# Kernel tuning notes

Measured on AMD Instinct MI355X. Metric: run time of the kernel, lower is better.

The kernel has to match this reference:

```python
import jax, jax.numpy as jnp
import numpy as np

B, D, N, S = 1024, 512, 500000, 32768


def setup_inputs() -> dict:
    key = jax.random.key(0)
    k1, k2, k3 = jax.random.split(key, 3)
    inputs = jax.random.normal(k1, (B, D), dtype=jnp.float32)
    # Linear(D, N) init: uniform(-0.05, 0.05) weight, zero bias
    weight = jax.random.uniform(k2, (N, D), dtype=jnp.float32, minval=-0.05, maxval=0.05)
    bias = jnp.zeros((N,), dtype=jnp.float32)
    sample_ids = jax.random.randint(k3, (S,), 0, N, dtype=jnp.int64)
    return {"inputs": inputs, "weight": weight, "bias": bias, "sample_ids": sample_ids}


def reference(inputs, weight, bias, sample_ids):
    # Gather retrieved class embeddings: [S, D] and their biases [S]
    sample_weights = weight[sample_ids]
    sample_bias = bias[sample_ids]
    # Sampled logits: inputs @ sample_weights.T + bias  -> [B, S]
    # (matches sample_weights.matmul(inputs.t()).t() + sample_bias in torch)
    logits = jnp.einsum("bd,sd->bs", inputs, sample_weights) + sample_bias
    return logits
```

## Files before the change

kernel.cpp:

```cpp
#include <hip/hip_runtime.h>
#include <stdint.h>

#define B_DIM 1024
#define D_DIM 512
#define S_DIM 32768

typedef __attribute__((ext_vector_type(8))) short bf16x8;
typedef __attribute__((ext_vector_type(4))) float f32x4;
typedef __attribute__((ext_vector_type(8))) unsigned short u16x8;

#define AS1 __attribute__((address_space(1)))
#define AS3 __attribute__((address_space(3)))

__device__ __forceinline__ unsigned short f2bf(float f) {
  union { float f; uint32_t u; } x; x.f = f;
  uint32_t r = x.u + 0x7fffu + ((x.u >> 16) & 1u);
  return (unsigned short)(r >> 16);
}

__global__ __launch_bounds__(256) void gather_w(const float* __restrict__ W,
                                                const float* __restrict__ bias,
                                                const int* __restrict__ ids,
                                                unsigned short* __restrict__ Wg,
                                                float* __restrict__ bg) {
  int gid = blockIdx.x * 256 + threadIdx.x;
  int s = gid >> 6;
  int c = (gid & 63) * 8;
  int sid = ids[s];
  const float* src = W + (size_t)sid * D_DIM + c;
  float4 v0 = *(const float4*)src;
  float4 v1 = *(const float4*)(src + 4);
  u16x8 o;
  o[0] = f2bf(v0.x); o[1] = f2bf(v0.y); o[2] = f2bf(v0.z); o[3] = f2bf(v0.w);
  o[4] = f2bf(v1.x); o[5] = f2bf(v1.y); o[6] = f2bf(v1.z); o[7] = f2bf(v1.w);
  *(u16x8*)(Wg + (size_t)s * D_DIM + c) = o;
  if ((gid & 63) == 0) bg[s] = bias[sid];
}

__global__ __launch_bounds__(256) void conv_a(const float* __restrict__ A,
                                              unsigned short* __restrict__ Ab) {
  int gid = blockIdx.x * 256 + threadIdx.x;
  const float* src = A + (size_t)gid * 8;
  float4 v0 = *(const float4*)src;
  float4 v1 = *(const float4*)(src + 4);
  u16x8 o;
  o[0] = f2bf(v0.x); o[1] = f2bf(v0.y); o[2] = f2bf(v0.z); o[3] = f2bf(v0.w);
  o[4] = f2bf(v1.x); o[5] = f2bf(v1.y); o[6] = f2bf(v1.z); o[7] = f2bf(v1.w);
  *(u16x8*)(Ab + (size_t)gid * 8) = o;
}

#define BM 256
#define BN 128
#define BK 64
#define NKT (D_DIM / BK)
#define ABYTES (BM * BK * 2)
#define BBYTES (BN * BK * 2)
#define BUFBYTES (ABYTES + BBYTES)

__global__ __launch_bounds__(512, 2) void gemm_bias(const unsigned short* __restrict__ Ab,
                                                    const unsigned short* __restrict__ Wg,
                                                    const float* __restrict__ bg,
                                                    float* __restrict__ out) {
  __shared__ __attribute__((aligned(16))) char lds[3 * BUFBYTES];

  const int tid = threadIdx.x;
  const int lane = tid & 63;
  const int w = tid >> 6;
  const int wr = w >> 1;
  const int wc = w & 1;
  const int lq = lane >> 4;
  const int l16 = lane & 15;

  int id = ((blockIdx.x & 7) << 7) | (blockIdx.x >> 3);
  const int bm = id & 3;
  const int bn = id >> 2;
  const int m0 = bm * BM;
  const int n0 = bn * BN;

  f32x4 acc[4][4];
#pragma unroll
  for (int m = 0; m < 4; ++m)
#pragma unroll
    for (int n = 0; n < 4; ++n)
      acc[m][n] = (f32x4)0.0f;

  auto stage = [&](int kt) {
    char* ldsA = lds + (kt % 3) * BUFBYTES;
    char* ldsB = ldsA + ABYTES;
#pragma unroll
    for (int j = 0; j < 4; ++j) {
      const int Pb = j * 8192 + w * 1024;
      const int P = Pb + lane * 16;
      const int L = P ^ (((P >> 7) & 7) << 4);
      const char* src = (const char*)Ab +
          (size_t)(m0 + (L >> 7)) * (D_DIM * 2) + kt * (BK * 2) + (L & 127);
      __builtin_amdgcn_global_load_lds((const AS1 void*)src,
                                       (AS3 void*)(ldsA + Pb), 16, 0, 0);
    }
#pragma unroll
    for (int j = 0; j < 2; ++j) {
      const int Pb = j * 8192 + w * 1024;
      const int P = Pb + lane * 16;
      const int L = P ^ (((P >> 7) & 7) << 4);
      const char* src = (const char*)Wg +
          (size_t)(n0 + (L >> 7)) * (D_DIM * 2) + kt * (BK * 2) + (L & 127);
      __builtin_amdgcn_global_load_lds((const AS1 void*)src,
                                       (AS3 void*)(ldsB + Pb), 16, 0, 0);
    }
  };

  stage(0);
  stage(1);

  const int swz = (l16 & 7) << 4;

#pragma unroll
  for (int kt = 0; kt < NKT; ++kt) {
    if (kt < NKT - 2) {
      stage(kt + 2);
      asm volatile("s_waitcnt vmcnt(12)" ::: "memory");
    } else if (kt == NKT - 2) {
      asm volatile("s_waitcnt vmcnt(6)" ::: "memory");
    } else {
      asm volatile("s_waitcnt vmcnt(0)" ::: "memory");
    }
    __builtin_amdgcn_s_barrier();
    __builtin_amdgcn_sched_barrier(0);

    const char* ldsA = lds + (kt % 3) * BUFBYTES;
    const char* ldsB = ldsA + ABYTES;

    bf16x8 af[2][4], bv[2][4];
#pragma unroll
    for (int kk = 0; kk < 2; ++kk) {
#pragma unroll
      for (int m = 0; m < 4; ++m) {
        const int row = wr * 64 + m * 16 + l16;
        const int byte = row * 128 + (kk * 32 + lq * 8) * 2;
        af[kk][m] = *(const bf16x8*)(ldsA + (byte ^ swz));
      }
#pragma unroll
      for (int n = 0; n < 4; ++n) {
        const int row = wc * 64 + n * 16 + l16;
        const int byte = row * 128 + (kk * 32 + lq * 8) * 2;
        bv[kk][n] = *(const bf16x8*)(ldsB + (byte ^ swz));
      }
    }

    __builtin_amdgcn_s_setprio(1);
#pragma unroll
    for (int kk = 0; kk < 2; ++kk)
#pragma unroll
      for (int m = 0; m < 4; ++m)
#pragma unroll
        for (int n = 0; n < 4; ++n)
          acc[m][n] = __builtin_amdgcn_mfma_f32_16x16x32_bf16(af[kk][m], bv[kk][n],
                                                              acc[m][n], 0, 0, 0);
    __builtin_amdgcn_s_setprio(0);

    __builtin_amdgcn_sched_barrier(0);
    __builtin_amdgcn_s_barrier();
  }

  const int lrow = lq * 4;
#pragma unroll
  for (int n = 0; n < 4; ++n) {
    const int col = n0 + wc * 64 + n * 16 + l16;
    const float bvv = bg[col];
#pragma unroll
    for (int m = 0; m < 4; ++m) {
      const int rbase = m0 + wr * 64 + m * 16 + lrow;
#pragma unroll
      for (int r = 0; r < 4; ++r) {
        out[(size_t)(rbase + r) * S_DIM + col] = acc[m][n][r] + bvv;
      }
    }
  }
}

extern "C" void kernel_launch(void* const* d_in, const int* in_sizes, int n_in,
                              void* d_out, int out_size, void* d_ws, size_t ws_size,
                              hipStream_t stream) {
  const float* inp  = (const float*)d_in[0];
  const float* W    = (const float*)d_in[1];
  const float* bias = (const float*)d_in[2];
  const int*   ids  = (const int*)d_in[3];
  float* out = (float*)d_out;

  unsigned short* Wg = (unsigned short*)d_ws;
  unsigned short* Ab = (unsigned short*)((char*)d_ws +
                        (size_t)S_DIM * D_DIM * 2);
  float* bg = (float*)((char*)d_ws +
                        (size_t)S_DIM * D_DIM * 2 + (size_t)B_DIM * D_DIM * 2);

  gather_w<<<S_DIM / 4, 256, 0, stream>>>(W, bias, ids, Wg, bg);
  conv_a<<<(B_DIM * D_DIM / 8) / 256, 256, 0, stream>>>(inp, Ab);

  dim3 grid((B_DIM / BM) * (S_DIM / BN));
  gemm_bias<<<grid, 512, 0, stream>>>(Ab, Wg, bg, out);
}
```

Measured before the change: 75.29 us.

## Fuse weight gather and bf16 conversion into GEMM B-tile loading

Removes the separate gather_w kernel and its bf16 staging buffer. Each GEMM block now loads its rows of W through ids straight into registers, converts them to bf16 and writes them into a double-buffered LDS tile. The bias is also read through ids in the epilogue. This saves one launch and the write/read round trip of the gathered weights. In exchange, fp32 weights are re-read by each of the 4 M-blocks, launch bounds drop to 1 block per SM, and the register-staged B path needs more waits and barriers.

New measurement: 82.12 us. +9.1%, slower.

```diff
diff --git a/kernel.cpp b/kernel.cpp
--- a/kernel.cpp
+++ b/kernel.cpp
@@ -17,24 +17,8 @@
   uint32_t r = x.u + 0x7fffu + ((x.u >> 16) & 1u);
   return (unsigned short)(r >> 16);
 }
-
-__global__ __launch_bounds__(256) void gather_w(const float* __restrict__ W,
-                                                const float* __restrict__ bias,
-                                                const int* __restrict__ ids,
-                                                unsigned short* __restrict__ Wg,
-                                                float* __restrict__ bg) {
-  int gid = blockIdx.x * 256 + threadIdx.x;
-  int s = gid >> 6;
-  int c = (gid & 63) * 8;
-  int sid = ids[s];
-  const float* src = W + (size_t)sid * D_DIM + c;
-  float4 v0 = *(const float4*)src;
-  float4 v1 = *(const float4*)(src + 4);
-  u16x8 o;
-  o[0] = f2bf(v0.x); o[1] = f2bf(v0.y); o[2] = f2bf(v0.z); o[3] = f2bf(v0.w);
-  o[4] = f2bf(v1.x); o[5] = f2bf(v1.y); o[6] = f2bf(v1.z); o[7] = f2bf(v1.w);
-  *(u16x8*)(Wg + (size_t)s * D_DIM + c) = o;
-  if ((gid & 63) == 0) bg[s] = bias[sid];
+__device__ __forceinline__ uint32_t pk2(float a, float b) {
+  return (uint32_t)f2bf(a) | ((uint32_t)f2bf(b) << 16);
 }
 
 __global__ __launch_bounds__(256) void conv_a(const float* __restrict__ A,
@@ -53,15 +37,16 @@
 #define BN 128
 #define BK 64
 #define NKT (D_DIM / BK)
-#define ABYTES (BM * BK * 2)
-#define BBYTES (BN * BK * 2)
-#define BUFBYTES (ABYTES + BBYTES)
-
-__global__ __launch_bounds__(512, 2) void gemm_bias(const unsigned short* __restrict__ Ab,
-                                                    const unsigned short* __restrict__ Wg,
-                                                    const float* __restrict__ bg,
-                                                    float* __restrict__ out) {
-  __shared__ __attribute__((aligned(16))) char lds[3 * BUFBYTES];
+#define A_BYTES (BM * BK * 2)
+#define B_BYTES (BN * BK * 2)
+
+__global__ __launch_bounds__(512, 1) void gemm_fused(const unsigned short* __restrict__ Ab,
+                                                     const float* __restrict__ W,
+                                                     const float* __restrict__ bias,
+                                                     const int* __restrict__ ids,
+                                                     float* __restrict__ out) {
+  __shared__ __attribute__((aligned(16))) char lds[3 * A_BYTES + 2 * B_BYTES];
+  char* ldsB0 = lds + 3 * A_BYTES;
 
   const int tid = threadIdx.x;
   const int lane = tid & 63;
@@ -77,6 +62,13 @@
   const int m0 = bm * BM;
   const int n0 = bn * BN;
 
+  const int srow = tid >> 2;
+  const int sseg = tid & 3;
+  const int myid = ids[n0 + srow];
+  const float* wbase = W + (size_t)myid * D_DIM + sseg * 16;
+  const int sbase = srow * 128 + sseg * 32;
+  const int sswz = (srow & 7) << 4;
+
   f32x4 acc[4][4];
 #pragma unroll
   for (int m = 0; m < 4; ++m)
@@ -84,9 +76,8 @@
     for (int n = 0; n < 4; ++n)
       acc[m][n] = (f32x4)0.0f;
 
-  auto stage = [&](int kt) {
-    char* ldsA = lds + (kt % 3) * BUFBYTES;
-    char* ldsB = ldsA + ABYTES;
+  auto stageA = [&](int kt) {
+    char* ldsA = lds + (kt % 3) * A_BYTES;
 #pragma unroll
     for (int j = 0; j < 4; ++j) {
       const int Pb = j * 8192 + w * 1024;
@@ -97,39 +88,52 @@
       __builtin_amdgcn_global_load_lds((const AS1 void*)src,
                                        (AS3 void*)(ldsA + Pb), 16, 0, 0);
     }
-#pragma unroll
-    for (int j = 0; j < 2; ++j) {
-      const int Pb = j * 8192 + w * 1024;
-      const int P = Pb + lane * 16;
-      const int L = P ^ (((P >> 7) & 7) << 4);
-      const char* src = (const char*)Wg +
-          (size_t)(n0 + (L >> 7)) * (D_DIM * 2) + kt * (BK * 2) + (L & 127);
-      __builtin_amdgcn_global_load_lds((const AS1 void*)src,
-                                       (AS3 void*)(ldsB + Pb), 16, 0, 0);
-    }
   };
 
-  stage(0);
-  stage(1);
+  float4 breg[2][4];
+
+  auto loadB = [&](int kt, int s) {
+    const float* p = wbase + kt * BK;
+    breg[s][0] = *(const float4*)(p + 0);
+    breg[s][1] = *(const float4*)(p + 4);
+    breg[s][2] = *(const float4*)(p + 8);
+    breg[s][3] = *(const float4*)(p + 12);
+  };
+  auto writeB = [&](int kt, int s) {
+    char* bb = ldsB0 + (kt & 1) * B_BYTES;
+    int4 w0, w1;
+    w0.x = pk2(breg[s][0].x, breg[s][0].y); w0.y = pk2(breg[s][0].z, breg[s][0].w);
+    w0.z = pk2(breg[s][1].x, breg[s][1].y); w0.w = pk2(breg[s][1].z, breg[s][1].w);
+    w1.x = pk2(breg[s][2].x, breg[s][2].y); w1.y = pk2(breg[s][2].z, breg[s][2].w);
+    w1.z = pk2(breg[s][3].x, breg[s][3].y); w1.w = pk2(breg[s][3].z, breg[s][3].w);
+    *(int4*)(bb + (sbase ^ sswz)) = w0;
+    *(int4*)(bb + ((sbase + 16) ^ sswz)) = w1;
+  };
+
+  loadB(0, 0);
+  stageA(0);
+  stageA(1);
+  asm volatile("s_waitcnt vmcnt(8)" ::: "memory");
+  writeB(0, 0);
+  loadB(1, 1);
+  asm volatile("s_waitcnt vmcnt(8)" ::: "memory");
+  asm volatile("s_waitcnt lgkmcnt(0)" ::: "memory");
+  __builtin_amdgcn_s_barrier();
 
   const int swz = (l16 & 7) << 4;
 
 #pragma unroll
   for (int kt = 0; kt < NKT; ++kt) {
-    if (kt < NKT - 2) {
-      stage(kt + 2);
-      asm volatile("s_waitcnt vmcnt(12)" ::: "memory");
-    } else if (kt == NKT - 2) {
-      asm volatile("s_waitcnt vmcnt(6)" ::: "memory");
-    } else {
-      asm volatile("s_waitcnt vmcnt(0)" ::: "memory");
-    }
-    __builtin_amdgcn_s_barrier();
     __builtin_amdgcn_sched_barrier(0);
-
-    const char* ldsA = lds + (kt % 3) * BUFBYTES;
-    const char* ldsB = ldsA + ABYTES;
-
+    if (kt <= NKT - 3) {
+      loadB(kt + 2, kt & 1);
+      __builtin_amdgcn_sched_barrier(0);
+      stageA(kt + 2);
+    }
+    __builtin_amdgcn_sched_barrier(0);
+
+    const char* ldsA = lds + (kt % 3) * A_BYTES;
+    const char* ldsB = ldsB0 + (kt & 1) * B_BYTES;
     bf16x8 af[2][4], bv[2][4];
 #pragma unroll
     for (int kk = 0; kk < 2; ++kk) {
@@ -157,16 +161,25 @@
           acc[m][n] = __builtin_amdgcn_mfma_f32_16x16x32_bf16(af[kk][m], bv[kk][n],
                                                               acc[m][n], 0, 0, 0);
     __builtin_amdgcn_s_setprio(0);
-
     __builtin_amdgcn_sched_barrier(0);
-    __builtin_amdgcn_s_barrier();
+
+    if (kt <= NKT - 2) {
+      if (kt <= NKT - 3)
+        asm volatile("s_waitcnt vmcnt(8)" ::: "memory");
+      else
+        asm volatile("s_waitcnt vmcnt(0)" ::: "memory");
+      writeB(kt + 1, (kt & 1) ^ 1);
+      __builtin_amdgcn_sched_barrier(0);
+      asm volatile("s_waitcnt lgkmcnt(0)" ::: "memory");
+      __builtin_amdgcn_s_barrier();
+    }
   }
 
   const int lrow = lq * 4;
 #pragma unroll
   for (int n = 0; n < 4; ++n) {
     const int col = n0 + wc * 64 + n * 16 + l16;
-    const float bvv = bg[col];
+    const float bvv = bias[ids[col]];
 #pragma unroll
     for (int m = 0; m < 4; ++m) {
       const int rbase = m0 + wr * 64 + m * 16 + lrow;
@@ -187,15 +200,10 @@
   const int*   ids  = (const int*)d_in[3];
   float* out = (float*)d_out;
 
-  unsigned short* Wg = (unsigned short*)d_ws;
-  unsigned short* Ab = (unsigned short*)((char*)d_ws +
-                        (size_t)S_DIM * D_DIM * 2);
-  float* bg = (float*)((char*)d_ws +
-                        (size_t)S_DIM * D_DIM * 2 + (size_t)B_DIM * D_DIM * 2);
-
-  gather_w<<<S_DIM / 4, 256, 0, stream>>>(W, bias, ids, Wg, bg);
+  unsigned short* Ab = (unsigned short*)d_ws;
+
   conv_a<<<(B_DIM * D_DIM / 8) / 256, 256, 0, stream>>>(inp, Ab);
 
   dim3 grid((B_DIM / BM) * (S_DIM / BN));
-  gemm_bias<<<grid, 512, 0, stream>>>(Ab, Wg, bg, out);
-}
+  gemm_fused<<<grid, 512, 0, stream>>>(Ab, W, bias, ids, out);
+}
```

## Shrink GEMM tile to 128x128 with 256 threads and double-buffered LDS

Applied to the files above, without the earlier changes.

Reduces the block tile from 256x128 with 8 waves to 128x128 with 4 waves, and changes the LDS pipeline from triple to double buffering with a one-stage prefetch. The grid doubles and the block-index swizzle is adjusted for 8 row tiles. The intent is less LDS per block and more blocks resident per CU for better latency hiding. In exchange each block reuses its W tile across fewer rows, so W is read from L2 more often, and the shallower prefetch exposes more load latency.

Result: faster. 64.93 us (-13.8%).

```diff
diff --git a/kernel.cpp b/kernel.cpp
--- a/kernel.cpp
+++ b/kernel.cpp
@@ -49,19 +49,19 @@
   *(u16x8*)(Ab + (size_t)gid * 8) = o;
 }
 
-#define BM 256
+#define BM 128
 #define BN 128
 #define BK 64
 #define NKT (D_DIM / BK)
-#define ABYTES (BM * BK * 2)
-#define BBYTES (BN * BK * 2)
-#define BUFBYTES (ABYTES + BBYTES)
+#define A_BYTES (BM * BK * 2)
+#define B_BYTES (BN * BK * 2)
+#define BUFBYTES (A_BYTES + B_BYTES)
 
-__global__ __launch_bounds__(512, 2) void gemm_bias(const unsigned short* __restrict__ Ab,
+__global__ __launch_bounds__(256, 2) void gemm_bias(const unsigned short* __restrict__ Ab,
                                                     const unsigned short* __restrict__ Wg,
                                                     const float* __restrict__ bg,
                                                     float* __restrict__ out) {
-  __shared__ __attribute__((aligned(16))) char lds[3 * BUFBYTES];
+  __shared__ __attribute__((aligned(16))) char lds[2 * BUFBYTES];
 
   const int tid = threadIdx.x;
   const int lane = tid & 63;
@@ -71,9 +71,9 @@
   const int lq = lane >> 4;
   const int l16 = lane & 15;
 
-  int id = ((blockIdx.x & 7) << 7) | (blockIdx.x >> 3);
-  const int bm = id & 3;
-  const int bn = id >> 2;
+  int id = ((blockIdx.x & 7) << 8) | (blockIdx.x >> 3);
+  const int bm = id & 7;
+  const int bn = id >> 3;
   const int m0 = bm * BM;
   const int n0 = bn * BN;
 
@@ -85,50 +85,43 @@
       acc[m][n] = (f32x4)0.0f;
 
   auto stage = [&](int kt) {
-    char* ldsA = lds + (kt % 3) * BUFBYTES;
-    char* ldsB = ldsA + ABYTES;
+    char* ldsA = lds + (kt & 1) * BUFBYTES;
+    char* ldsB = ldsA + A_BYTES;
 #pragma unroll
     for (int j = 0; j < 4; ++j) {
-      const int Pb = j * 8192 + w * 1024;
+      const int Pb = j * 4096 + w * 1024;
       const int P = Pb + lane * 16;
       const int L = P ^ (((P >> 7) & 7) << 4);
-      const char* src = (const char*)Ab +
+      const char* srcA = (const char*)Ab +
           (size_t)(m0 + (L >> 7)) * (D_DIM * 2) + kt * (BK * 2) + (L & 127);
-      __builtin_amdgcn_global_load_lds((const AS1 void*)src,
+      __builtin_amdgcn_global_load_lds((const AS1 void*)srcA,
                                        (AS3 void*)(ldsA + Pb), 16, 0, 0);
-    }
-#pragma unroll
-    for (int j = 0; j < 2; ++j) {
-      const int Pb = j * 8192 + w * 1024;
-      const int P = Pb + lane * 16;
-      const int L = P ^ (((P >> 7) & 7) << 4);
-      const char* src = (const char*)Wg +
+      const char* srcB = (const char*)Wg +
           (size_t)(n0 + (L >> 7)) * (D_DIM * 2) + kt * (BK * 2) + (L & 127);
-      __builtin_amdgcn_global_load_lds((const AS1 void*)src,
+      __builtin_amdgcn_global_load_lds((const AS1 void*)srcB,
                                        (AS3 void*)(ldsB + Pb), 16, 0, 0);
     }
   };
 
   stage(0);
-  stage(1);
 
   const int swz = (l16 & 7) << 4;
 
 #pragma unroll
   for (int kt = 0; kt < NKT; ++kt) {
-    if (kt < NKT - 2) {
-      stage(kt + 2);
-      asm volatile("s_waitcnt vmcnt(12)" ::: "memory");
-    } else if (kt == NKT - 2) {
-      asm volatile("s_waitcnt vmcnt(6)" ::: "memory");
+    __builtin_amdgcn_sched_barrier(0);
+    if (kt < NKT - 1) {
+      stage(kt + 1);
+      __builtin_amdgcn_sched_barrier(0);
+      asm volatile("s_waitcnt vmcnt(8)" ::: "memory");
     } else {
       asm volatile("s_waitcnt vmcnt(0)" ::: "memory");
     }
     __builtin_amdgcn_s_barrier();
     __builtin_amdgcn_sched_barrier(0);
 
-    const char* ldsA = lds + (kt % 3) * BUFBYTES;
-    const char* ldsB = ldsA + ABYTES;
+    const char* ldsA = lds + (kt & 1) * BUFBYTES;
+    const char* ldsB = ldsA + A_BYTES;
 
     bf16x8 af[2][4], bv[2][4];
 #pragma unroll
@@ -197,5 +190,5 @@
   conv_a<<<(B_DIM * D_DIM / 8) / 256, 256, 0, stream>>>(inp, Ab);
 
   dim3 grid((B_DIM / BM) * (S_DIM / BN));
-  gemm_bias<<<grid, 512, 0, stream>>>(Ab, Wg, bg, out);
+  gemm_bias<<<grid, 256, 0, stream>>>(Ab, Wg, bg, out);
 }
```
